# Optimization experiments

Measured on AMD Instinct MI355X. Metric: run time of the kernel, lower is better.

## Reference

```python
import jax, jax.numpy as jnp
import numpy as np
import math

N_HEADS = 16
D_HEAD = 64
D_MODEL = 1024
ROPE_THETA = 10000.0


def setup_inputs() -> dict:
    key = jax.random.key(0)
    k1, k2, k3 = jax.random.split(key, 3)
    B, T = 2, 2048
    x = jax.random.normal(k1, (B, T, D_MODEL), dtype=jnp.float32)
    # torch Linear(in, out) weight has shape (out, in); store transposed (in, out)
    # so forward is x @ w. Scale like default init to keep activations sane.
    w_qkv = jax.random.normal(k2, (D_MODEL, 3 * D_MODEL), dtype=jnp.float32) / math.sqrt(D_MODEL)
    w_o = jax.random.normal(k3, (D_MODEL, D_MODEL), dtype=jnp.float32) / math.sqrt(D_MODEL)
    return {"x": x, "w_qkv": w_qkv, "w_o": w_o}


def _build_rope(T, dtype):
    inv_freq = 1.0 / (ROPE_THETA ** (jnp.arange(0, D_HEAD, 2, dtype=jnp.float32) / D_HEAD))
    t = jnp.arange(T, dtype=jnp.float32)
    freqs = jnp.outer(t, inv_freq)            # [T, D_HEAD/2]
    emb = jnp.concatenate([freqs, freqs], -1)  # [T, D_HEAD]
    return jnp.cos(emb).astype(dtype), jnp.sin(emb).astype(dtype)


def _apply_rope(x, cos, sin):
    # x: [B, T, H, D_HEAD]; cos/sin broadcast as [1, T, 1, D_HEAD]
    x1, x2 = jnp.split(x, 2, axis=-1)
    rotated = jnp.concatenate([-x2, x1], axis=-1)
    return x * cos + rotated * sin


def reference(x, w_qkv, w_o):
    B, T, D = x.shape
    qkv = (x @ w_qkv).reshape(B, T, 3, N_HEADS, D_HEAD)
    q, k, v = qkv[:, :, 0], qkv[:, :, 1], qkv[:, :, 2]  # [B, T, H, Dh]
    cos, sin = _build_rope(T, x.dtype)
    cos = cos[None, :, None, :]
    sin = sin[None, :, None, :]
    q = _apply_rope(q, cos, sin)
    k = _apply_rope(k, cos, sin)
    scale = 1.0 / math.sqrt(D_HEAD)
    # full [B, H, T, T] scores (faithful to the manual matmul-softmax-matmul)
    attn = jnp.einsum("bthd,bshd->bhts", q, k) * scale
    attn = jax.nn.softmax(attn, axis=-1)
    out = jnp.einsum("bhts,bshd->bthd", attn, v).reshape(B, T, D)
    return out @ w_o
```

## Files before the change

### kernel.cpp

```cpp
#include <hip/hip_runtime.h>
#include <cstdint>

typedef unsigned short ushort_t;
typedef __attribute__((ext_vector_type(8))) short v8s;
typedef __attribute__((ext_vector_type(4))) short v4s;
typedef __attribute__((ext_vector_type(2))) unsigned v2u;
typedef __attribute__((ext_vector_type(4))) float v4f;

#define MFMA(a, b, c) __builtin_amdgcn_mfma_f32_16x16x32_bf16(a, b, c, 0, 0, 0)

__device__ __forceinline__ float bf2f(ushort_t u) {
    union { unsigned u; float f; } x; x.u = ((unsigned)u) << 16; return x.f;
}
__device__ __forceinline__ short f2bf(float f) {
    union { float f; unsigned u; } x; x.f = f;
    unsigned r = x.u + 0x7fffu + ((x.u >> 16) & 1u);
    return (short)(r >> 16);
}

__global__ void detect_dtype(const unsigned* __restrict__ x, int* __restrict__ flag) {
    __shared__ int cnt;
    if (threadIdx.x == 0) cnt = 0;
    __syncthreads();
    unsigned w = x[threadIdx.x];
    int e = (w >> 7) & 0xFF;
    int hit = ((e >= 96 && e <= 135) || (w & 0xFFFFu) == 0) ? 1 : 0;
    atomicAdd(&cnt, hit);
    __syncthreads();
    if (threadIdx.x == 0) *flag = (cnt >= 160) ? 1 : 0;
}

__global__ __launch_bounds__(256) void cvt_x(const void* __restrict__ xin,
                                             ushort_t* __restrict__ xb,
                                             const int* __restrict__ flagp, int n8) {
    int i = blockIdx.x * 256 + threadIdx.x;
    if (i >= n8) return;
    if (*flagp) {
        ((v8s*)xb)[i] = ((const v8s*)xin)[i];
    } else {
        const float* xf = (const float*)xin + (size_t)i * 8;
        v8s o;
        #pragma unroll
        for (int j = 0; j < 8; ++j) o[j] = f2bf(xf[j]);
        ((v8s*)xb)[i] = o;
    }
}

__global__ __launch_bounds__(256) void cvt_transpose(const void* __restrict__ in,
                                                     ushort_t* __restrict__ out,
                                                     const int* __restrict__ flagp,
                                                     int R, int C) {
    __shared__ ushort_t tile[32][33];
    int bx = blockIdx.x * 32, by = blockIdx.y * 32;
    int tx = threadIdx.x, ty = threadIdx.y;
    int isbf = *flagp;
    for (int i = ty; i < 32; i += 8) {
        size_t idx = (size_t)(by + i) * C + bx + tx;
        tile[i][tx] = isbf ? ((const ushort_t*)in)[idx]
                           : (ushort_t)f2bf(((const float*)in)[idx]);
    }
    __syncthreads();
    for (int i = ty; i < 32; i += 8) out[(size_t)(bx + i) * R + by + tx] = tile[tx][i];
}

template <int OUTMODE>
__global__ __launch_bounds__(256) void gemm_bt(const ushort_t* __restrict__ A,
                                               const ushort_t* __restrict__ BT,
                                               void* __restrict__ C,
                                               const int* __restrict__ flagp,
                                               int M, int N, int K) {
    __shared__ __align__(16) ushort_t As[128 * 32];
    __shared__ __align__(16) ushort_t Bs[128 * 32];
    int tid = threadIdx.x;
    int lane = tid & 63;
    int lr = lane & 15, lc = lane >> 4;
    int w = tid >> 6;
    int wr = (w >> 1) * 64, wc = (w & 1) * 64;
    int m0 = blockIdx.y * 128, n0 = blockIdx.x * 128;

    int c0 = tid, c1 = tid + 256;
    int r0 = c0 >> 2, s0 = c0 & 3;
    int r1 = c1 >> 2, s1 = c1 & 3;

    v4f acc[4][4] = {};

    for (int kt = 0; kt < K; kt += 32) {
        v8s a0 = *(const v8s*)(A + (size_t)(m0 + r0) * K + kt + s0 * 8);
        v8s a1 = *(const v8s*)(A + (size_t)(m0 + r1) * K + kt + s1 * 8);
        v8s b0 = *(const v8s*)(BT + (size_t)(n0 + r0) * K + kt + s0 * 8);
        v8s b1 = *(const v8s*)(BT + (size_t)(n0 + r1) * K + kt + s1 * 8);
        __syncthreads();
        *(v8s*)(As + (size_t)c0 * 8) = a0;
        *(v8s*)(As + (size_t)c1 * 8) = a1;
        *(v8s*)(Bs + (size_t)c0 * 8) = b0;
        *(v8s*)(Bs + (size_t)c1 * 8) = b1;
        __syncthreads();

        v8s af[4], bfr[4];
        #pragma unroll
        for (int i = 0; i < 4; ++i)
            af[i] = *(const v8s*)(As + (wr + i * 16 + lr) * 32 + lc * 8);
        #pragma unroll
        for (int j = 0; j < 4; ++j)
            bfr[j] = *(const v8s*)(Bs + (wc + j * 16 + lr) * 32 + lc * 8);
        #pragma unroll
        for (int i = 0; i < 4; ++i)
            #pragma unroll
            for (int j = 0; j < 4; ++j)
                acc[i][j] = MFMA(af[i], bfr[j], acc[i][j]);
    }
    int store_f32 = (OUTMODE == 1) && (*flagp == 0);
    #pragma unroll
    for (int i = 0; i < 4; ++i)
        #pragma unroll
        for (int j = 0; j < 4; ++j)
            #pragma unroll
            for (int r = 0; r < 4; ++r) {
                int row = m0 + wr + i * 16 + lc * 4 + r;
                int col = n0 + wc + j * 16 + lr;
                if (store_f32)
                    ((float*)C)[(size_t)row * N + col] = acc[i][j][r];
                else
                    ((ushort_t*)C)[(size_t)row * N + col] = (ushort_t)f2bf(acc[i][j][r]);
            }
}

__global__ __launch_bounds__(256) void rope_table(float* __restrict__ tab) {
    int idx = blockIdx.x * 256 + threadIdx.x;
    int t = idx >> 5, d = idx & 31;
    float inv_freq = __expf(-(float)d * 0.28782313662425575f);
    float ang = (float)t * inv_freq;
    float sn, cs;
    sincosf(ang, &sn, &cs);
    tab[t * 64 + d]      = bf2f((ushort_t)f2bf(cs));
    tab[t * 64 + 32 + d] = bf2f((ushort_t)f2bf(sn));
}

#define QSCALE 0.18033688011112042f
__global__ __launch_bounds__(256) void rope_reshape(const ushort_t* __restrict__ qkv,
                                                    const float* __restrict__ tab,
                                                    ushort_t* __restrict__ Qr,
                                                    ushort_t* __restrict__ Kr,
                                                    ushort_t* __restrict__ Vt) {
    __shared__ __align__(16) ushort_t Vl[64][72];
    int tid = threadIdx.x;
    int tq = tid >> 2, dc = tid & 3;
    int t0 = blockIdx.x * 64;
    int bh = blockIdx.y;
    int b = bh >> 4, h = bh & 15;
    int t = t0 + tq;
    size_t rb = ((size_t)(b * 2048 + t)) * 3072 + h * 64;

    v8s qlo = *(const v8s*)(qkv + rb + dc * 8);
    v8s qhi = *(const v8s*)(qkv + rb + dc * 8 + 32);
    v8s klo = *(const v8s*)(qkv + rb + 1024 + dc * 8);
    v8s khi = *(const v8s*)(qkv + rb + 1024 + dc * 8 + 32);
    v8s vlo = *(const v8s*)(qkv + rb + 2048 + dc * 8);
    v8s vhi = *(const v8s*)(qkv + rb + 2048 + dc * 8 + 32);

    const float* ct = tab + t * 64 + dc * 8;
    v8s qolo, qohi, kolo, kohi;
    #pragma unroll
    for (int j = 0; j < 8; ++j) {
        float cb = ct[j], sb = ct[32 + j];
        float x1 = bf2f((ushort_t)qlo[j]), x2 = bf2f((ushort_t)qhi[j]);
        qolo[j] = f2bf((x1 * cb - x2 * sb) * QSCALE);
        qohi[j] = f2bf((x2 * cb + x1 * sb) * QSCALE);
        float k1 = bf2f((ushort_t)klo[j]), k2 = bf2f((ushort_t)khi[j]);
        kolo[j] = f2bf(k1 * cb - k2 * sb);
        kohi[j] = f2bf(k2 * cb + k1 * sb);
    }
    size_t ob = ((size_t)bh * 2048 + t) * 64;
    *(v8s*)(Qr + ob + dc * 8) = qolo;
    *(v8s*)(Qr + ob + dc * 8 + 32) = qohi;
    *(v8s*)(Kr + ob + dc * 8) = kolo;
    *(v8s*)(Kr + ob + dc * 8 + 32) = kohi;

    *(v8s*)(&Vl[tq][dc * 8]) = vlo;
    *(v8s*)(&Vl[tq][dc * 8 + 32]) = vhi;
    __syncthreads();
    int d = tid >> 2, tc = tid & 3;
    v8s o1, o2;
    #pragma unroll
    for (int k = 0; k < 8; ++k) o1[k] = (short)Vl[tc * 16 + k][d];
    #pragma unroll
    for (int k = 0; k < 8; ++k) o2[k] = (short)Vl[tc * 16 + 8 + k][d];
    size_t vb = (size_t)bh * 131072 + (size_t)((t0 >> 5) + (tc >> 1)) * 2048
              + d * 32 + (tc & 1) * 16;
    *(v8s*)(Vt + vb) = o1;
    *(v8s*)(Vt + vb + 8) = o2;
}

__global__ __launch_bounds__(128) void attn(const ushort_t* __restrict__ Qr,
                                            const ushort_t* __restrict__ Kr,
                                            const ushort_t* __restrict__ Vt,
                                            ushort_t* __restrict__ AO) {
    __shared__ __align__(16) ushort_t P[2 * 2560];
    __shared__ __align__(16) float MO[64 * 68];
    __shared__ float Mli[64];
    int tid = threadIdx.x, lane = tid & 63, W = tid >> 6;
    int lr = lane & 15, lc = lane >> 4;
    int L = blockIdx.x;
    int xcd = L & 7, slot = L >> 3;
    int bh = xcd * 4 + (slot >> 5);
    int q0 = (slot & 31) * 64;
    int b = bh >> 4, h = bh & 15;
    const ushort_t* Qb = Qr + ((size_t)bh * 2048 + q0) * 64;
    const ushort_t* Kp = Kr + (size_t)bh * 131072 + (size_t)W * 65536 + lr * 64 + lc * 8;
    const ushort_t* Vp = Vt + (size_t)bh * 131072 + (size_t)W * 65536 + lr * 32 + lc * 8;
    ushort_t* Pw = P + W * 2560;

    v8s qf[4][2];
    #pragma unroll
    for (int jq = 0; jq < 4; ++jq)
        #pragma unroll
        for (int kk = 0; kk < 2; ++kk)
            qf[jq][kk] = *(const v8s*)(Qb + (size_t)(jq * 16 + lr) * 64 + kk * 32 + lc * 8);

    v4f o[4][4] = {};
    float li[4] = {0.f, 0.f, 0.f, 0.f};

    auto loadK = [&](v8s (&kf)[2][2], int stp) {
        #pragma unroll
        for (int hh = 0; hh < 2; ++hh)
            #pragma unroll
            for (int kk = 0; kk < 2; ++kk)
                kf[hh][kk] = *(const v8s*)(Kp + (size_t)stp * 2048 + hh * 1024 + kk * 32);
    };
    auto loadV = [&](v8s (&vf)[4], int stp) {
        #pragma unroll
        for (int i = 0; i < 4; ++i)
            vf[i] = *(const v8s*)(Vp + (size_t)stp * 2048 + i * 512);
    };
    auto step = [&](v8s (&kf)[2][2], v8s (&vf)[4]) {
        v4f St[2][4] = {};
        #pragma unroll
        for (int hh = 0; hh < 2; ++hh)
            #pragma unroll
            for (int jq = 0; jq < 4; ++jq) {
                St[hh][jq] = MFMA(kf[hh][0], qf[jq][0], St[hh][jq]);
                St[hh][jq] = MFMA(kf[hh][1], qf[jq][1], St[hh][jq]);
            }
        #pragma unroll
        for (int jq = 0; jq < 4; ++jq) {
            #pragma unroll
            for (int hh = 0; hh < 2; ++hh) {
                #pragma unroll
                for (int r = 0; r < 4; ++r) {
                    float ev = __builtin_amdgcn_exp2f(St[hh][jq][r]);
                    St[hh][jq][r] = ev;
                    li[jq] += ev;
                }
                unsigned d0 = __builtin_amdgcn_perm(__float_as_uint(St[hh][jq][1]),
                                                    __float_as_uint(St[hh][jq][0]), 0x07060302u);
                unsigned d1 = __builtin_amdgcn_perm(__float_as_uint(St[hh][jq][3]),
                                                    __float_as_uint(St[hh][jq][2]), 0x07060302u);
                v2u pk = {d0, d1};
                *(v2u*)(Pw + (jq * 16 + lr) * 40 + hh * 16 + lc * 4) = pk;
            }
        }
        __builtin_amdgcn_s_waitcnt(0xc07f);
        #pragma unroll
        for (int jq = 0; jq < 4; ++jq) {
            v8s pf = *(const v8s*)(Pw + (jq * 16 + lr) * 40 + lc * 8);
            #pragma unroll
            for (int i = 0; i < 4; ++i)
                o[i][jq] = MFMA(vf[i], pf, o[i][jq]);
        }
    };

    v8s kfA[2][2], vfA[4], kfB[2][2], vfB[4];
    loadK(kfA, 0);
    loadV(vfA, 0);
    for (int stp = 0; stp < 32; stp += 2) {
        loadK(kfB, stp + 1);
        loadV(vfB, stp + 1);
        step(kfA, vfA);
        if (stp + 2 < 32) {
            loadK(kfA, stp + 2);
            loadV(vfA, stp + 2);
        }
        step(kfB, vfB);
    }

    #pragma unroll
    for (int jq = 0; jq < 4; ++jq) {
        li[jq] += __shfl_xor(li[jq], 16);
        li[jq] += __shfl_xor(li[jq], 32);
    }
    if (W == 1) {
        #pragma unroll
        for (int jq = 0; jq < 4; ++jq) {
            #pragma unroll
            for (int i = 0; i < 4; ++i)
                *(v4f*)(MO + (jq * 16 + lr) * 68 + i * 16 + lc * 4) = o[i][jq];
            if (lc == 0) Mli[jq * 16 + lr] = li[jq];
        }
    }
    __syncthreads();
    if (W == 0) {
        #pragma unroll
        for (int jq = 0; jq < 4; ++jq) {
            float inv = 1.0f / (li[jq] + Mli[jq * 16 + lr]);
            int t = q0 + jq * 16 + lr;
            #pragma unroll
            for (int i = 0; i < 4; ++i) {
                v4f m = *(const v4f*)(MO + (jq * 16 + lr) * 68 + i * 16 + lc * 4);
                v4s pk;
                #pragma unroll
                for (int r = 0; r < 4; ++r) pk[r] = f2bf((o[i][jq][r] + m[r]) * inv);
                *(v4s*)(AO + (size_t)(b * 2048 + t) * 1024 + h * 64 + i * 16 + lc * 4) = pk;
            }
        }
    }
}

extern "C" void kernel_launch(void* const* d_in, const int* in_sizes, int n_in,
                              void* d_out, int out_size, void* d_ws, size_t ws_size,
                              hipStream_t stream) {
    char* ws = (char*)d_ws;
    int*      flag  = (int*)ws;
    ushort_t* wqkvT = (ushort_t*)(ws + 256);
    ushort_t* woT   = (ushort_t*)(ws + 6291712);
    ushort_t* xb    = (ushort_t*)(ws + 8388864);
    ushort_t* qkv   = (ushort_t*)(ws + 16777472);
    ushort_t* Qr    = (ushort_t*)(ws + 41943296);
    ushort_t* Vt    = (ushort_t*)(ws + 50331904);
    float*    tab   = (float*)(ws + 58720512);
    ushort_t* Kr    = xb;
    ushort_t* AO    = qkv;

    detect_dtype<<<1, 256, 0, stream>>>((const unsigned*)d_in[0], flag);
    rope_table<<<256, 256, 0, stream>>>(tab);
    cvt_x<<<2048, 256, 0, stream>>>(d_in[0], xb, flag, 524288);
    dim3 tb(32, 8);
    cvt_transpose<<<dim3(96, 32), tb, 0, stream>>>(d_in[1], wqkvT, flag, 1024, 3072);
    cvt_transpose<<<dim3(32, 32), tb, 0, stream>>>(d_in[2], woT, flag, 1024, 1024);
    gemm_bt<0><<<dim3(24, 32), 256, 0, stream>>>(xb, wqkvT, qkv, flag, 4096, 3072, 1024);
    rope_reshape<<<dim3(32, 32), 256, 0, stream>>>(qkv, tab, Qr, Kr, Vt);
    attn<<<1024, 128, 0, stream>>>(Qr, Kr, Vt, AO);
    gemm_bt<1><<<dim3(8, 32), 256, 0, stream>>>(AO, woT, d_out, flag, 4096, 1024, 1024);
}
```

Measured before the change: 228.1 us.

## Split attention KV across four waves with XCC-aware dynamic work queue

The attention block grows from two to four waves, each handling a quarter of the key/value sequence, and the partial outputs are combined through a two-level LDS reduction. Work items are claimed dynamically via per-XCD atomic counters read from the hardware XCC id, which keeps each (batch, head) on one XCD for L2 reuse. The inner loop is software-pipelined so QK of the next tile overlaps exp/pack and PV of the current tile, using double-buffered P in LDS. In exchange it adds reduction syncs, an extra memset and atomics, and more register and LDS pressure per block.

```diff
diff --git a/kernel.cpp b/kernel.cpp
--- a/kernel.cpp
+++ b/kernel.cpp
@@ -191,24 +191,39 @@
     *(v8s*)(Vt + vb + 8) = o2;
 }
 
-__global__ __launch_bounds__(128) void attn(const ushort_t* __restrict__ Qr,
-                                            const ushort_t* __restrict__ Kr,
-                                            const ushort_t* __restrict__ Vt,
-                                            ushort_t* __restrict__ AO) {
-    __shared__ __align__(16) ushort_t P[2 * 2560];
-    __shared__ __align__(16) float MO[64 * 68];
-    __shared__ float Mli[64];
+__global__ __launch_bounds__(256, 3) void attn(const ushort_t* __restrict__ Qr,
+                                               const ushort_t* __restrict__ Kr,
+                                               const ushort_t* __restrict__ Vt,
+                                               ushort_t* __restrict__ AO,
+                                               int* __restrict__ ctr) {
+    __shared__ __align__(16) ushort_t P[4 * 2 * 2560];
+    __shared__ float LiA[64], LiB[64];
+    __shared__ int s_item;
     int tid = threadIdx.x, lane = tid & 63, W = tid >> 6;
     int lr = lane & 15, lc = lane >> 4;
-    int L = blockIdx.x;
-    int xcd = L & 7, slot = L >> 3;
-    int bh = xcd * 4 + (slot >> 5);
-    int q0 = (slot & 31) * 64;
+
+    unsigned xcc;
+    asm volatile("s_getreg_b32 %0, hwreg(20, 0, 4)" : "=s"(xcc));
+    if (tid == 0) {
+        int item = -1;
+        #pragma unroll 1
+        for (int j = 0; j < 8; ++j) {
+            int x = ((int)xcc + j) & 7;
+            int idx = atomicAdd(&ctr[x], 1);
+            if (idx < 128) { item = x * 128 + idx; break; }
+        }
+        s_item = item;
+    }
+    __syncthreads();
+    int item = s_item;
+    if (item < 0) return;
+    int bh = item >> 5;
+    int q0 = (item & 31) * 64;
     int b = bh >> 4, h = bh & 15;
+
     const ushort_t* Qb = Qr + ((size_t)bh * 2048 + q0) * 64;
-    const ushort_t* Kp = Kr + (size_t)bh * 131072 + (size_t)W * 65536 + lr * 64 + lc * 8;
-    const ushort_t* Vp = Vt + (size_t)bh * 131072 + (size_t)W * 65536 + lr * 32 + lc * 8;
-    ushort_t* Pw = P + W * 2560;
+    const ushort_t* Kp = Kr + (size_t)bh * 131072 + (size_t)W * 32768 + lr * 64 + lc * 8;
+    const ushort_t* Vp = Vt + (size_t)bh * 131072 + (size_t)W * 32768 + lr * 32 + lc * 8;
 
     v8s qf[4][2];
     #pragma unroll
@@ -232,34 +247,36 @@
         for (int i = 0; i < 4; ++i)
             vf[i] = *(const v8s*)(Vp + (size_t)stp * 2048 + i * 512);
     };
-    auto step = [&](v8s (&kf)[2][2], v8s (&vf)[4]) {
-        v4f St[2][4] = {};
+    auto qk = [&](v4f (&S)[2][4], v8s (&kf)[2][2]) {
         #pragma unroll
         for (int hh = 0; hh < 2; ++hh)
             #pragma unroll
             for (int jq = 0; jq < 4; ++jq) {
-                St[hh][jq] = MFMA(kf[hh][0], qf[jq][0], St[hh][jq]);
-                St[hh][jq] = MFMA(kf[hh][1], qf[jq][1], St[hh][jq]);
-            }
-        #pragma unroll
-        for (int jq = 0; jq < 4; ++jq) {
+                v4f z = {0.f, 0.f, 0.f, 0.f};
+                z = MFMA(kf[hh][0], qf[jq][0], z);
+                S[hh][jq] = MFMA(kf[hh][1], qf[jq][1], z);
+            }
+    };
+    auto exp_pack = [&](v4f (&S)[2][4], ushort_t* Pw) {
+        #pragma unroll
+        for (int jq = 0; jq < 4; ++jq)
             #pragma unroll
             for (int hh = 0; hh < 2; ++hh) {
                 #pragma unroll
                 for (int r = 0; r < 4; ++r) {
-                    float ev = __builtin_amdgcn_exp2f(St[hh][jq][r]);
-                    St[hh][jq][r] = ev;
+                    float ev = __builtin_amdgcn_exp2f(S[hh][jq][r]);
+                    S[hh][jq][r] = ev;
                     li[jq] += ev;
                 }
-                unsigned d0 = __builtin_amdgcn_perm(__float_as_uint(St[hh][jq][1]),
-                                                    __float_as_uint(St[hh][jq][0]), 0x07060302u);
-                unsigned d1 = __builtin_amdgcn_perm(__float_as_uint(St[hh][jq][3]),
-                                                    __float_as_uint(St[hh][jq][2]), 0x07060302u);
+                unsigned d0 = __builtin_amdgcn_perm(__float_as_uint(S[hh][jq][1]),
+                                                    __float_as_uint(S[hh][jq][0]), 0x07060302u);
+                unsigned d1 = __builtin_amdgcn_perm(__float_as_uint(S[hh][jq][3]),
+                                                    __float_as_uint(S[hh][jq][2]), 0x07060302u);
                 v2u pk = {d0, d1};
                 *(v2u*)(Pw + (jq * 16 + lr) * 40 + hh * 16 + lc * 4) = pk;
             }
-        }
-        __builtin_amdgcn_s_waitcnt(0xc07f);
+    };
+    auto pv = [&](ushort_t* Pw, v8s (&vf)[4]) {
         #pragma unroll
         for (int jq = 0; jq < 4; ++jq) {
             v8s pf = *(const v8s*)(Pw + (jq * 16 + lr) * 40 + lc * 8);
@@ -269,18 +286,22 @@
         }
     };
 
-    v8s kfA[2][2], vfA[4], kfB[2][2], vfB[4];
-    loadK(kfA, 0);
-    loadV(vfA, 0);
-    for (int stp = 0; stp < 32; stp += 2) {
-        loadK(kfB, stp + 1);
-        loadV(vfB, stp + 1);
-        step(kfA, vfA);
-        if (stp + 2 < 32) {
-            loadK(kfA, stp + 2);
-            loadV(vfA, stp + 2);
-        }
-        step(kfB, vfB);
+    v8s kb[2][2][2], vb[2][4];
+    v4f Sb[2][2][4];
+    loadK(kb[0], 0); loadV(vb[0], 0);
+    loadK(kb[1], 1); loadV(vb[1], 1);
+    qk(Sb[0], kb[0]);
+
+    #pragma unroll
+    for (int t = 0; t < 16; ++t) {
+        int p = t & 1, pn = p ^ 1;
+        ushort_t* Pw = P + (W * 2 + p) * 2560;
+        if (t + 2 < 16) loadK(kb[p], t + 2);
+        exp_pack(Sb[p], Pw);
+        if (t + 1 < 16) qk(Sb[pn], kb[pn]);
+        __builtin_amdgcn_s_waitcnt(0xc07f);
+        pv(Pw, vb[p]);
+        if (t + 2 < 16) loadV(vb[p], t + 2);
     }
 
     #pragma unroll
@@ -288,24 +309,54 @@
         li[jq] += __shfl_xor(li[jq], 16);
         li[jq] += __shfl_xor(li[jq], 32);
     }
-    if (W == 1) {
+    float* bufA = (float*)P;
+    float* bufB = (float*)((char*)P + 17408);
+    __syncthreads();
+    if (W == 1 || W == 3) {
+        float* buf = (W == 1) ? bufA : bufB;
+        float* Lb  = (W == 1) ? LiA : LiB;
         #pragma unroll
         for (int jq = 0; jq < 4; ++jq) {
             #pragma unroll
             for (int i = 0; i < 4; ++i)
-                *(v4f*)(MO + (jq * 16 + lr) * 68 + i * 16 + lc * 4) = o[i][jq];
-            if (lc == 0) Mli[jq * 16 + lr] = li[jq];
+                *(v4f*)(buf + (jq * 16 + lr) * 68 + i * 16 + lc * 4) = o[i][jq];
+            if (lc == 0) Lb[jq * 16 + lr] = li[jq];
+        }
+    }
+    __syncthreads();
+    if (W == 0 || W == 2) {
+        float* buf = (W == 0) ? bufA : bufB;
+        float* Lb  = (W == 0) ? LiA : LiB;
+        #pragma unroll
+        for (int jq = 0; jq < 4; ++jq) {
+            li[jq] += Lb[jq * 16 + lr];
+            #pragma unroll
+            for (int i = 0; i < 4; ++i) {
+                v4f m = *(const v4f*)(buf + (jq * 16 + lr) * 68 + i * 16 + lc * 4);
+                #pragma unroll
+                for (int r = 0; r < 4; ++r) o[i][jq][r] += m[r];
+            }
+        }
+    }
+    __syncthreads();
+    if (W == 2) {
+        #pragma unroll
+        for (int jq = 0; jq < 4; ++jq) {
+            #pragma unroll
+            for (int i = 0; i < 4; ++i)
+                *(v4f*)(bufA + (jq * 16 + lr) * 68 + i * 16 + lc * 4) = o[i][jq];
+            if (lc == 0) LiA[jq * 16 + lr] = li[jq];
         }
     }
     __syncthreads();
     if (W == 0) {
         #pragma unroll
         for (int jq = 0; jq < 4; ++jq) {
-            float inv = 1.0f / (li[jq] + Mli[jq * 16 + lr]);
+            float inv = 1.0f / (li[jq] + LiA[jq * 16 + lr]);
             int t = q0 + jq * 16 + lr;
             #pragma unroll
             for (int i = 0; i < 4; ++i) {
-                v4f m = *(const v4f*)(MO + (jq * 16 + lr) * 68 + i * 16 + lc * 4);
+                v4f m = *(const v4f*)(bufA + (jq * 16 + lr) * 68 + i * 16 + lc * 4);
                 v4s pk;
                 #pragma unroll
                 for (int r = 0; r < 4; ++r) pk[r] = f2bf((o[i][jq][r] + m[r]) * inv);
@@ -320,6 +371,7 @@
                               hipStream_t stream) {
     char* ws = (char*)d_ws;
     int*      flag  = (int*)ws;
+    int*      ctr   = (int*)(ws + 64);
     ushort_t* wqkvT = (ushort_t*)(ws + 256);
     ushort_t* woT   = (ushort_t*)(ws + 6291712);
     ushort_t* xb    = (ushort_t*)(ws + 8388864);
@@ -330,6 +382,7 @@
     ushort_t* Kr    = xb;
     ushort_t* AO    = qkv;
 
+    hipMemsetAsync(ctr, 0, 32, stream);
     detect_dtype<<<1, 256, 0, stream>>>((const unsigned*)d_in[0], flag);
     rope_table<<<256, 256, 0, stream>>>(tab);
     cvt_x<<<2048, 256, 0, stream>>>(d_in[0], xb, flag, 524288);
@@ -338,6 +391,6 @@
     cvt_transpose<<<dim3(32, 32), tb, 0, stream>>>(d_in[2], woT, flag, 1024, 1024);
     gemm_bt<0><<<dim3(24, 32), 256, 0, stream>>>(xb, wqkvT, qkv, flag, 4096, 3072, 1024);
     rope_reshape<<<dim3(32, 32), 256, 0, stream>>>(qkv, tab, Qr, Kr, Vt);
-    attn<<<1024, 128, 0, stream>>>(Qr, Kr, Vt, AO);
+    attn<<<1024, 256, 0, stream>>>(Qr, Kr, Vt, AO, ctr);
     gemm_bt<1><<<dim3(8, 32), 256, 0, stream>>>(AO, woT, d_out, flag, 4096, 1024, 1024);
 }
```

Result: slower. 497.5 us (+118.1%).

## Fuse RoPE and Q/K/V relayout into QKV GEMM epilogue; asm-pipelined attention loads

Applied to the files above, without the earlier changes.

The QKV GEMM epilogue now applies RoPE and the Q scale, and writes Q, K and transposed V straight into the head-major layouts attention expects. This removes the separate rope_reshape kernel and the round trip of the qkv intermediate through global memory. Separately, the attention K/V prefetch becomes inline-asm global loads into a two-slot register buffer with explicit vmcnt waits, so loads stay in flight across a step. The epilogue now uses scattered 2-byte stores for Q/K, and the asm waits depend on exact vmcnt accounting.

```diff
diff --git a/kernel.cpp b/kernel.cpp
--- a/kernel.cpp
+++ b/kernel.cpp
@@ -8,6 +8,7 @@
 typedef __attribute__((ext_vector_type(4))) float v4f;
 
 #define MFMA(a, b, c) __builtin_amdgcn_mfma_f32_16x16x32_bf16(a, b, c, 0, 0, 0)
+#define QSCALE 0.18033688011112042f
 
 __device__ __forceinline__ float bf2f(ushort_t u) {
     union { unsigned u; float f; } x; x.u = ((unsigned)u) << 16; return x.f;
@@ -63,12 +64,27 @@
     for (int i = ty; i < 32; i += 8) out[(size_t)(bx + i) * R + by + tx] = tile[tx][i];
 }
 
-template <int OUTMODE>
+__global__ __launch_bounds__(256) void rope_table(float* __restrict__ tab) {
+    int idx = blockIdx.x * 256 + threadIdx.x;
+    int t = idx >> 5, d = idx & 31;
+    float inv_freq = __expf(-(float)d * 0.28782313662425575f);
+    float ang = (float)t * inv_freq;
+    float sn, cs;
+    sincosf(ang, &sn, &cs);
+    tab[t * 64 + d]      = bf2f((ushort_t)f2bf(cs));
+    tab[t * 64 + 32 + d] = bf2f((ushort_t)f2bf(sn));
+}
+
+template <int MODE>
 __global__ __launch_bounds__(256) void gemm_bt(const ushort_t* __restrict__ A,
                                                const ushort_t* __restrict__ BT,
                                                void* __restrict__ C,
                                                const int* __restrict__ flagp,
-                                               int M, int N, int K) {
+                                               int M, int N, int K,
+                                               ushort_t* __restrict__ Qp,
+                                               ushort_t* __restrict__ Kp,
+                                               ushort_t* __restrict__ Vp,
+                                               const float* __restrict__ tab) {
     __shared__ __align__(16) ushort_t As[128 * 32];
     __shared__ __align__(16) ushort_t Bs[128 * 32];
     int tid = threadIdx.x;
@@ -109,87 +125,73 @@
             for (int j = 0; j < 4; ++j)
                 acc[i][j] = MFMA(af[i], bfr[j], acc[i][j]);
     }
-    int store_f32 = (OUTMODE == 1) && (*flagp == 0);
-    #pragma unroll
-    for (int i = 0; i < 4; ++i)
-        #pragma unroll
-        for (int j = 0; j < 4; ++j)
-            #pragma unroll
-            for (int r = 0; r < 4; ++r) {
-                int row = m0 + wr + i * 16 + lc * 4 + r;
-                int col = n0 + wc + j * 16 + lr;
-                if (store_f32)
-                    ((float*)C)[(size_t)row * N + col] = acc[i][j][r];
-                else
-                    ((ushort_t*)C)[(size_t)row * N + col] = (ushort_t)f2bf(acc[i][j][r]);
-            }
-}
-
-__global__ __launch_bounds__(256) void rope_table(float* __restrict__ tab) {
-    int idx = blockIdx.x * 256 + threadIdx.x;
-    int t = idx >> 5, d = idx & 31;
-    float inv_freq = __expf(-(float)d * 0.28782313662425575f);
-    float ang = (float)t * inv_freq;
-    float sn, cs;
-    sincosf(ang, &sn, &cs);
-    tab[t * 64 + d]      = bf2f((ushort_t)f2bf(cs));
-    tab[t * 64 + 32 + d] = bf2f((ushort_t)f2bf(sn));
-}
-
-#define QSCALE 0.18033688011112042f
-__global__ __launch_bounds__(256) void rope_reshape(const ushort_t* __restrict__ qkv,
-                                                    const float* __restrict__ tab,
-                                                    ushort_t* __restrict__ Qr,
-                                                    ushort_t* __restrict__ Kr,
-                                                    ushort_t* __restrict__ Vt) {
-    __shared__ __align__(16) ushort_t Vl[64][72];
-    int tid = threadIdx.x;
-    int tq = tid >> 2, dc = tid & 3;
-    int t0 = blockIdx.x * 64;
-    int bh = blockIdx.y;
-    int b = bh >> 4, h = bh & 15;
-    int t = t0 + tq;
-    size_t rb = ((size_t)(b * 2048 + t)) * 3072 + h * 64;
-
-    v8s qlo = *(const v8s*)(qkv + rb + dc * 8);
-    v8s qhi = *(const v8s*)(qkv + rb + dc * 8 + 32);
-    v8s klo = *(const v8s*)(qkv + rb + 1024 + dc * 8);
-    v8s khi = *(const v8s*)(qkv + rb + 1024 + dc * 8 + 32);
-    v8s vlo = *(const v8s*)(qkv + rb + 2048 + dc * 8);
-    v8s vhi = *(const v8s*)(qkv + rb + 2048 + dc * 8 + 32);
-
-    const float* ct = tab + t * 64 + dc * 8;
-    v8s qolo, qohi, kolo, kohi;
-    #pragma unroll
-    for (int j = 0; j < 8; ++j) {
-        float cb = ct[j], sb = ct[32 + j];
-        float x1 = bf2f((ushort_t)qlo[j]), x2 = bf2f((ushort_t)qhi[j]);
-        qolo[j] = f2bf((x1 * cb - x2 * sb) * QSCALE);
-        qohi[j] = f2bf((x2 * cb + x1 * sb) * QSCALE);
-        float k1 = bf2f((ushort_t)klo[j]), k2 = bf2f((ushort_t)khi[j]);
-        kolo[j] = f2bf(k1 * cb - k2 * sb);
-        kohi[j] = f2bf(k2 * cb + k1 * sb);
-    }
-    size_t ob = ((size_t)bh * 2048 + t) * 64;
-    *(v8s*)(Qr + ob + dc * 8) = qolo;
-    *(v8s*)(Qr + ob + dc * 8 + 32) = qohi;
-    *(v8s*)(Kr + ob + dc * 8) = kolo;
-    *(v8s*)(Kr + ob + dc * 8 + 32) = kohi;
-
-    *(v8s*)(&Vl[tq][dc * 8]) = vlo;
-    *(v8s*)(&Vl[tq][dc * 8 + 32]) = vhi;
-    __syncthreads();
-    int d = tid >> 2, tc = tid & 3;
-    v8s o1, o2;
-    #pragma unroll
-    for (int k = 0; k < 8; ++k) o1[k] = (short)Vl[tc * 16 + k][d];
-    #pragma unroll
-    for (int k = 0; k < 8; ++k) o2[k] = (short)Vl[tc * 16 + 8 + k][d];
-    size_t vb = (size_t)bh * 131072 + (size_t)((t0 >> 5) + (tc >> 1)) * 2048
-              + d * 32 + (tc & 1) * 16;
-    *(v8s*)(Vt + vb) = o1;
-    *(v8s*)(Vt + vb + 8) = o2;
-}
+
+    if (MODE == 1) {
+        int store_f32 = (*flagp == 0);
+        #pragma unroll
+        for (int i = 0; i < 4; ++i)
+            #pragma unroll
+            for (int j = 0; j < 4; ++j)
+                #pragma unroll
+                for (int r = 0; r < 4; ++r) {
+                    int row = m0 + wr + i * 16 + lc * 4 + r;
+                    int col = n0 + wc + j * 16 + lr;
+                    if (store_f32)
+                        ((float*)C)[(size_t)row * N + col] = acc[i][j][r];
+                    else
+                        ((ushort_t*)C)[(size_t)row * N + col] = (ushort_t)f2bf(acc[i][j][r]);
+                }
+    } else {
+        int region = n0 >> 10;
+        int h = ((n0 & 1023) + wc) >> 6;
+        if (region < 2) {
+            const float sc = (region == 0) ? QSCALE : 1.0f;
+            ushort_t* dst = (region == 0) ? Qp : Kp;
+            #pragma unroll
+            for (int i = 0; i < 4; ++i)
+                #pragma unroll
+                for (int j = 0; j < 2; ++j) {
+                    int d = j * 16 + lr;
+                    #pragma unroll
+                    for (int r = 0; r < 4; ++r) {
+                        int tg = m0 + wr + i * 16 + lc * 4 + r;
+                        int b = tg >> 11, tt = tg & 2047;
+                        float cs = tab[tt * 64 + d], sn = tab[tt * 64 + 32 + d];
+                        float x1 = acc[i][j][r], x2 = acc[i][j + 2][r];
+                        size_t base = ((size_t)(b * 16 + h) * 2048 + tt) * 64 + d;
+                        dst[base]      = (ushort_t)f2bf((x1 * cs - x2 * sn) * sc);
+                        dst[base + 32] = (ushort_t)f2bf((x2 * cs + x1 * sn) * sc);
+                    }
+                }
+        } else {
+            #pragma unroll
+            for (int i = 0; i < 4; ++i)
+                #pragma unroll
+                for (int j = 0; j < 4; ++j) {
+                    int d = j * 16 + lr;
+                    int tg0 = m0 + wr + i * 16 + lc * 4;
+                    int b = tg0 >> 11, tt = tg0 & 2047;
+                    v4s pk;
+                    #pragma unroll
+                    for (int r = 0; r < 4; ++r) pk[r] = f2bf(acc[i][j][r]);
+                    size_t base = (size_t)(b * 16 + h) * 131072 + (size_t)(tt >> 5) * 2048
+                                + (size_t)d * 32 + (tt & 31);
+                    *(v4s*)(Vp + base) = pk;
+                }
+        }
+    }
+}
+
+#define ISSUE_LOAD(dst, ptr) \
+    asm volatile("global_load_dwordx4 %0, %1, off" : "=v"(dst) : "v"(ptr))
+#define WAIT_VM8(sl) \
+    asm volatile("s_waitcnt vmcnt(8)" \
+        : "+v"(kf[sl][0][0]), "+v"(kf[sl][0][1]), "+v"(kf[sl][1][0]), "+v"(kf[sl][1][1]), \
+          "+v"(vf[sl][0]), "+v"(vf[sl][1]), "+v"(vf[sl][2]), "+v"(vf[sl][3]))
+#define WAIT_VM0(sl) \
+    asm volatile("s_waitcnt vmcnt(0)" \
+        : "+v"(kf[sl][0][0]), "+v"(kf[sl][0][1]), "+v"(kf[sl][1][0]), "+v"(kf[sl][1][1]), \
+          "+v"(vf[sl][0]), "+v"(vf[sl][1]), "+v"(vf[sl][2]), "+v"(vf[sl][3]))
 
 __global__ __launch_bounds__(128) void attn(const ushort_t* __restrict__ Qr,
                                             const ushort_t* __restrict__ Kr,
@@ -219,30 +221,37 @@
 
     v4f o[4][4] = {};
     float li[4] = {0.f, 0.f, 0.f, 0.f};
-
-    auto loadK = [&](v8s (&kf)[2][2], int stp) {
+    v8s kf[2][2][2], vf[2][4];
+
+    auto issueK = [&](int sl, int stp) {
         #pragma unroll
         for (int hh = 0; hh < 2; ++hh)
             #pragma unroll
-            for (int kk = 0; kk < 2; ++kk)
-                kf[hh][kk] = *(const v8s*)(Kp + (size_t)stp * 2048 + hh * 1024 + kk * 32);
+            for (int kk = 0; kk < 2; ++kk) {
+                const ushort_t* p = Kp + (size_t)stp * 2048 + hh * 1024 + kk * 32;
+                if (sl == 0) ISSUE_LOAD(kf[0][hh][kk], p);
+                else         ISSUE_LOAD(kf[1][hh][kk], p);
+            }
     };
-    auto loadV = [&](v8s (&vf)[4], int stp) {
-        #pragma unroll
-        for (int i = 0; i < 4; ++i)
-            vf[i] = *(const v8s*)(Vp + (size_t)stp * 2048 + i * 512);
+    auto issueV = [&](int sl, int stp) {
+        #pragma unroll
+        for (int i = 0; i < 4; ++i) {
+            const ushort_t* p = Vp + (size_t)stp * 2048 + i * 512;
+            if (sl == 0) ISSUE_LOAD(vf[0][i], p);
+            else         ISSUE_LOAD(vf[1][i], p);
+        }
     };
-    auto step = [&](v8s (&kf)[2][2], v8s (&vf)[4]) {
+    auto step = [&](v8s (&kfs)[2][2], v8s (&vfs)[4]) {
         v4f St[2][4] = {};
         #pragma unroll
         for (int hh = 0; hh < 2; ++hh)
             #pragma unroll
             for (int jq = 0; jq < 4; ++jq) {
-                St[hh][jq] = MFMA(kf[hh][0], qf[jq][0], St[hh][jq]);
-                St[hh][jq] = MFMA(kf[hh][1], qf[jq][1], St[hh][jq]);
+                St[hh][jq] = MFMA(kfs[hh][0], qf[jq][0], St[hh][jq]);
+                St[hh][jq] = MFMA(kfs[hh][1], qf[jq][1], St[hh][jq]);
             }
         #pragma unroll
-        for (int jq = 0; jq < 4; ++jq) {
+        for (int jq = 0; jq < 4; ++jq)
             #pragma unroll
             for (int hh = 0; hh < 2; ++hh) {
                 #pragma unroll
@@ -258,29 +267,26 @@
                 v2u pk = {d0, d1};
                 *(v2u*)(Pw + (jq * 16 + lr) * 40 + hh * 16 + lc * 4) = pk;
             }
-        }
         __builtin_amdgcn_s_waitcnt(0xc07f);
         #pragma unroll
         for (int jq = 0; jq < 4; ++jq) {
             v8s pf = *(const v8s*)(Pw + (jq * 16 + lr) * 40 + lc * 8);
             #pragma unroll
             for (int i = 0; i < 4; ++i)
-                o[i][jq] = MFMA(vf[i], pf, o[i][jq]);
+                o[i][jq] = MFMA(vfs[i], pf, o[i][jq]);
         }
     };
 
-    v8s kfA[2][2], vfA[4], kfB[2][2], vfB[4];
-    loadK(kfA, 0);
-    loadV(vfA, 0);
+    issueK(0, 0); issueV(0, 0);
+    issueK(1, 1); issueV(1, 1);
+    #pragma unroll 1
     for (int stp = 0; stp < 32; stp += 2) {
-        loadK(kfB, stp + 1);
-        loadV(vfB, stp + 1);
-        step(kfA, vfA);
-        if (stp + 2 < 32) {
-            loadK(kfA, stp + 2);
-            loadV(vfA, stp + 2);
-        }
-        step(kfB, vfB);
+        WAIT_VM8(0);
+        step(kf[0], vf[0]);
+        if (stp + 2 < 32) { issueK(0, stp + 2); issueV(0, stp + 2); }
+        if (stp + 3 < 32) { WAIT_VM8(1); } else { WAIT_VM0(1); }
+        step(kf[1], vf[1]);
+        if (stp + 3 < 32) { issueK(1, stp + 3); issueV(1, stp + 3); }
     }
 
     #pragma unroll
@@ -323,12 +329,11 @@
     ushort_t* wqkvT = (ushort_t*)(ws + 256);
     ushort_t* woT   = (ushort_t*)(ws + 6291712);
     ushort_t* xb    = (ushort_t*)(ws + 8388864);
-    ushort_t* qkv   = (ushort_t*)(ws + 16777472);
-    ushort_t* Qr    = (ushort_t*)(ws + 41943296);
-    ushort_t* Vt    = (ushort_t*)(ws + 50331904);
-    float*    tab   = (float*)(ws + 58720512);
-    ushort_t* Kr    = xb;
-    ushort_t* AO    = qkv;
+    ushort_t* Qr    = (ushort_t*)(ws + 16777472);
+    ushort_t* Kr    = (ushort_t*)(ws + 25166080);
+    ushort_t* Vt    = (ushort_t*)(ws + 33554688);
+    ushort_t* AO    = (ushort_t*)(ws + 41943296);
+    float*    tab   = (float*)(ws + 50331904);
 
     detect_dtype<<<1, 256, 0, stream>>>((const unsigned*)d_in[0], flag);
     rope_table<<<256, 256, 0, stream>>>(tab);
@@ -336,8 +341,9 @@
     dim3 tb(32, 8);
     cvt_transpose<<<dim3(96, 32), tb, 0, stream>>>(d_in[1], wqkvT, flag, 1024, 3072);
     cvt_transpose<<<dim3(32, 32), tb, 0, stream>>>(d_in[2], woT, flag, 1024, 1024);
-    gemm_bt<0><<<dim3(24, 32), 256, 0, stream>>>(xb, wqkvT, qkv, flag, 4096, 3072, 1024);
-    rope_reshape<<<dim3(32, 32), 256, 0, stream>>>(qkv, tab, Qr, Kr, Vt);
+    gemm_bt<2><<<dim3(24, 32), 256, 0, stream>>>(xb, wqkvT, nullptr, flag, 4096, 3072, 1024,
+                                                 Qr, Kr, Vt, tab);
     attn<<<1024, 128, 0, stream>>>(Qr, Kr, Vt, AO);
-    gemm_bt<1><<<dim3(8, 32), 256, 0, stream>>>(AO, woT, d_out, flag, 4096, 1024, 1024);
-}
+    gemm_bt<1><<<dim3(8, 32), 256, 0, stream>>>(AO, woT, d_out, flag, 4096, 1024, 1024,
+                                                nullptr, nullptr, nullptr, nullptr);
+}
```

Result: faster. 217.4 us (-4.7%).
